# Kernel optimization log

Hardware: AMD Instinct MI355X
Metric: run time of the kernel (lower is better)

The kernel has to match this reference:

```python
import jax, jax.numpy as jnp
import numpy as np

DT = 0.05        # Euler step size
S_EULER = 2      # Euler steps between consecutive events, and after the last one (prop_to_end)


def setup_inputs() -> dict:
    key = jax.random.key(0)
    B, H, D, K, E = 512, 512, 128, 64, 256
    ks = jax.random.split(key, 16)

    def w(k, fan_in, fan_out):
        return jax.random.normal(k, (fan_in, fan_out), jnp.float32) / np.float32(np.sqrt(fan_in))

    X = jax.random.normal(ks[0], (K, E, D), jnp.float32)
    M = jax.random.bernoulli(ks[1], 0.5, (K, E, D)).astype(jnp.float32)
    # unique sample indices per event (irregular observation pattern, no scatter collisions)
    batch_idx = jax.vmap(lambda k: jax.random.permutation(k, B)[:E])(jax.random.split(ks[2], K))
    sample_idx = jnp.arange(B)
    b = lambda n: jnp.full((n,), 0.01, jnp.float32)  # torch init: bias filled with 0.01
    return {
        'X': X, 'M': M, 'batch_idx': batch_idx, 'sample_idx': sample_idx,
        'Wi': w(ks[3], D + H, H), 'bi': b(H),
        'Wf': w(ks[4], D + H, H), 'bf': b(H),
        'Wo': w(ks[5], D + H, H), 'bo': b(H),
        'Wc': w(ks[6], D + H, H), 'bc': b(H),
        'W1': w(ks[7], H, H), 'b1': b(H),
        'W2': w(ks[8], H, H), 'b2': b(H),
        'Wp1': w(ks[9], H, H), 'bp1': b(H),
        'Wp2': w(ks[10], H, D), 'bp2': b(D),
    }


def reference(X, M, batch_idx, sample_idx,
              Wi, bi, Wf, bf, Wo, bo, Wc, bc,
              W1, b1, W2, b2, Wp1, bp1, Wp2, bp2):
    B = sample_idx.shape[0]
    H = W1.shape[0]
    h0 = jnp.zeros((B, H), X.dtype)
    c0 = jnp.zeros((B, H), X.dtype)

    def euler(h):  # h <- h + dt * ODEFunc(h)
        return h + DT * (jnp.tanh(h @ W1 + b1) @ W2 + b2)

    def p_model(h):  # Linear -> ReLU -> (Dropout p=0, eval) -> Linear
        return jax.nn.relu(h @ Wp1 + bp1) @ Wp2 + bp2

    def step(carry, xs):
        h, c, loss, tot_m = carry
        Xo, Mo, idx = xs  # [E,D], [E,D], [E]
        for _ in range(S_EULER):
            h = euler(h)
        p = p_model(h)
        loss = loss + jnp.sum(jnp.abs(Xo - p[idx]) * Mo)
        tot_m = tot_m + jnp.sum(Mo)
        inp = jnp.concatenate([Xo, h[idx]], axis=-1)  # [E, D+H]
        ig = jax.nn.sigmoid(inp @ Wi + bi)
        fg = jax.nn.sigmoid(inp @ Wf + bf)
        og = jax.nn.sigmoid(inp @ Wo + bo)
        ct = jnp.tanh(inp @ Wc + bc)
        c_new = fg * c[idx] + ig * ct
        h_new = og * jnp.tanh(c_new)
        return (h.at[idx].set(h_new), c.at[idx].set(c_new), loss, tot_m), None

    init = (h0, c0, jnp.float32(0.0), jnp.float32(0.0))
    (h, c, loss, tot_m), _ = jax.lax.scan(step, init, (X, M, batch_idx))
    for _ in range(S_EULER):  # prop_to_end up to T
        h = euler(h)
    return jnp.stack([loss, loss / tot_m])
```

## Files before the change

kernel.cpp:

```cpp
#include <hip/hip_runtime.h>
#include <hip/hip_fp16.h>
#include <stdint.h>

#define Kn 64
#define En 256
#define Bn 512
#define Hn 512
#define Dn 128
#define NBLK 256
#define NTH  256
#define DT_C 0.05f


typedef _Float16 f16x8 __attribute__((ext_vector_type(8)));
typedef float    f32x4 __attribute__((ext_vector_type(4)));
typedef unsigned long long u64;

__device__ __forceinline__ float sigm(float x){ return 1.0f/(1.0f + __expf(-x)); }

__device__ __forceinline__ u64 ald(const u64* p){
  return __hip_atomic_load(p, __ATOMIC_RELAXED, __HIP_MEMORY_SCOPE_AGENT);
}
__device__ __forceinline__ void ast(u64* p, u64 v){
  __hip_atomic_store(p, v, __ATOMIC_RELAXED, __HIP_MEMORY_SCOPE_AGENT);
}

union HU { __half h[8]; u64 q[2]; uint32_t w[4]; };

__global__ void k_init(int* __restrict__ pos, float* __restrict__ acc,
                       int* __restrict__ ctr, uint32_t* __restrict__ hf){
  int i = blockIdx.x*blockDim.x + threadIdx.x;
  if (i < Kn*Bn) pos[i] = -1;
  if (i < 2) acc[i] = 0.0f;
  if (i < 1024) ctr[i] = 0;
  if (i < Hn*Hn/2) hf[i] = 0;
}

__global__ void k_scatter(const int* __restrict__ bidx, int* __restrict__ pos){
  int i = blockIdx.x*blockDim.x + threadIdx.x;
  if (i < Kn*En){
    int k = i >> 8;
    int e = i & (En-1);
    pos[(k << 9) | bidx[i]] = e;
  }
}

__global__ void k_cvt_frag(const float* __restrict__ src, __half* __restrict__ dst,
                           int KT, int N, int n){
  int i = blockIdx.x*blockDim.x + threadIdx.x;
  if (i >= n) return;
  int C = i / (KT*512);
  int r = i % (KT*512);
  int T = r >> 9;
  int q = r & 511;
  int l = q >> 3, e = q & 7;
  int srow = T*32 + ((l>>4)<<3) + e;
  int scol = C*16 + (l&15);
  dst[i] = __float2half(src[(size_t)srow*N + scol]);
}

__device__ __forceinline__ void gsync(int* c, int tgt){
  asm volatile("s_waitcnt vmcnt(0)" ::: "memory");
  __syncthreads();
  if (threadIdx.x == 0){
    __hip_atomic_fetch_add(c, 1, __ATOMIC_RELAXED, __HIP_MEMORY_SCOPE_AGENT);
    while (__hip_atomic_load(c, __ATOMIC_RELAXED, __HIP_MEMORY_SCOPE_AGENT) < tgt)
      __builtin_amdgcn_s_sleep(1);
  }
  __syncthreads();
}

__global__ __launch_bounds__(NTH, 1) void k_main(
  const float* __restrict__ X, const float* __restrict__ Mm,
  const int* __restrict__ pos, const __half* __restrict__ WF,
  __half* __restrict__ Hf, __half* __restrict__ Tf,
  const float* __restrict__ bi_, const float* __restrict__ bf_,
  const float* __restrict__ bo_, const float* __restrict__ bc_,
  const float* __restrict__ b1_, const float* __restrict__ b2_,
  const float* __restrict__ bp1_, const float* __restrict__ bp2_,
  float* __restrict__ acc, int* __restrict__ ctrbase)
{
  const __half* W1F  = WF;
  const __half* W2F  = WF + 262144;
  const __half* Wp1F = WF + 524288;
  const __half* Wp2F = WF + 786432;
  const __half* WgF  = WF + 851968;

  const int t    = threadIdx.x;
  const int bid  = blockIdx.x;
  const int s    = bid & 7;
  const int g    = bid >> 3;
  const int w    = t >> 6;
  const int lane = t & 63;

  int* ctr = ctrbase + g*32;

  __shared__ __align__(16) __half Afrag[16*512];
  __shared__ __align__(16) __half Xfrag[4*512];
  __shared__ __align__(16) float  outb[20*256];
  __shared__ float redbuf[8];

  const int row = t >> 4;
  const int q4  = t & 15;
  const int sc  = s*64 + q4*4;
  float Hreg[4] = {0,0,0,0};
  float Creg[4] = {0,0,0,0};
  float vb1[4], vb2[4], vbp1[4], vbi[4], vbf[4], vbo[4], vbc[4];
  #pragma unroll
  for (int i=0;i<4;i++){
    vb1[i]=b1_[sc+i]; vb2[i]=b2_[sc+i]; vbp1[i]=bp1_[sc+i];
    vbi[i]=bi_[sc+i]; vbf[i]=bf_[sc+i]; vbo[i]=bo_[sc+i]; vbc[i]=bc_[sc+i];
  }
  const float vbp2 = bp2_[s*16 + q4];

  f16x8 W1r[16], W2r[16], Wp1r[16];
  {
    const size_t cb = (size_t)(s*4 + w)*16*512 + lane*8;
    #pragma unroll
    for (int kt=0; kt<16; kt++){
      W1r[kt]  = *(const f16x8*)(W1F  + cb + kt*512);
      W2r[kt]  = *(const f16x8*)(W2F  + cb + kt*512);
      Wp1r[kt] = *(const f16x8*)(Wp1F + cb + kt*512);
    }
  }

  float loss_loc = 0.f, m_loc = 0.f;
  int round = 0;
  const int grow = g*16 + row;

  for (int k=0; k<Kn; k++){
    const int epos = pos[(k<<9) + grow];

    #pragma unroll 1
    for (int ph=0; ph<4; ph++){
      const __half* src = (ph & 1) ? Tf : Hf;
      {
        const int ar = t & 15, ch = t >> 4;
        const u64* sp = (const u64*)(src + ((size_t)(g*16+ar))*512 + ch*32);
        u64 v[8];
        #pragma unroll
        for (int i=0;i<8;i++) v[i] = ald(sp+i);
        #pragma unroll
        for (int kg=0;kg<4;kg++){
          u64* d = (u64*)(Afrag + ch*512 + (ar + 16*kg)*8);
          d[0] = v[2*kg]; d[1] = v[2*kg+1];
        }
      }
      __syncthreads();
      {
        f32x4 a4 = {0,0,0,0};
        if (!(ph & 1)){
          #pragma unroll
          for (int kt=0; kt<16; kt++){
            f16x8 a = *(const f16x8*)(Afrag + kt*512 + lane*8);
            a4 = __builtin_amdgcn_mfma_f32_16x16x32_f16(a, W1r[kt], a4, 0,0,0);
          }
        } else {
          #pragma unroll
          for (int kt=0; kt<16; kt++){
            f16x8 a = *(const f16x8*)(Afrag + kt*512 + lane*8);
            a4 = __builtin_amdgcn_mfma_f32_16x16x32_f16(a, W2r[kt], a4, 0,0,0);
          }
        }
        float* o = outb + w*256 + ((lane>>4)*4)*16 + (lane&15);
        o[0]=a4[0]; o[16]=a4[1]; o[32]=a4[2]; o[48]=a4[3];
      }
      __syncthreads();
      {
        const float* o = outb + (q4>>2)*256 + row*16 + (q4&3)*4;
        float v0=o[0], v1=o[1], v2=o[2], v3=o[3];
        HU u;
        if (!(ph & 1)){
          u.h[0]=__float2half(tanhf(v0+vb1[0])); u.h[1]=__float2half(tanhf(v1+vb1[1]));
          u.h[2]=__float2half(tanhf(v2+vb1[2])); u.h[3]=__float2half(tanhf(v3+vb1[3]));
          ast((u64*)(Tf + (size_t)grow*512 + sc), u.q[0]);
        } else {
          Hreg[0] += DT_C*(v0+vb2[0]); Hreg[1] += DT_C*(v1+vb2[1]);
          Hreg[2] += DT_C*(v2+vb2[2]); Hreg[3] += DT_C*(v3+vb2[3]);
          u.h[0]=__float2half(Hreg[0]); u.h[1]=__float2half(Hreg[1]);
          u.h[2]=__float2half(Hreg[2]); u.h[3]=__float2half(Hreg[3]);
          ast((u64*)(Hf + (size_t)grow*512 + sc), u.q[0]);
        }
      }
      gsync(ctr, 8*(++round));
    }

    {
      {
        const int ar = t & 15, ch = t >> 4;
        const u64* sp = (const u64*)(Hf + ((size_t)(g*16+ar))*512 + ch*32);
        u64 v[8];
        #pragma unroll
        for (int i=0;i<8;i++) v[i] = ald(sp+i);
        #pragma unroll
        for (int kg=0;kg<4;kg++){
          u64* d = (u64*)(Afrag + ch*512 + (ar + 16*kg)*8);
          d[0] = v[2*kg]; d[1] = v[2*kg+1];
        }
      }
      if (t < 64){
        const int ar = t & 15, ch = t >> 4;
        const int e = pos[(k<<9) + g*16 + ar];
        float xv[32];
        if (e >= 0){
          const float4* xp = (const float4*)(X + ((size_t)(k*En+e))*Dn + ch*32);
          #pragma unroll
          for (int i=0;i<8;i++){
            float4 f = xp[i];
            xv[4*i]=f.x; xv[4*i+1]=f.y; xv[4*i+2]=f.z; xv[4*i+3]=f.w;
          }
        } else {
          #pragma unroll
          for (int i=0;i<32;i++) xv[i]=0.f;
        }
        #pragma unroll
        for (int kg=0;kg<4;kg++){
          HU u;
          #pragma unroll
          for (int e8=0;e8<8;e8++) u.h[e8] = __float2half(xv[kg*8+e8]);
          u64* d = (u64*)(Xfrag + ch*512 + (ar + 16*kg)*8);
          d[0] = u.q[0]; d[1] = u.q[1];
        }
      }
      __syncthreads();
      {
        f32x4 a4 = {0,0,0,0};
        #pragma unroll
        for (int kt=0; kt<16; kt++){
          f16x8 a = *(const f16x8*)(Afrag + kt*512 + lane*8);
          a4 = __builtin_amdgcn_mfma_f32_16x16x32_f16(a, Wp1r[kt], a4, 0,0,0);
        }
        float* o = outb + (16+w)*256 + ((lane>>4)*4)*16 + (lane&15);
        o[0]=a4[0]; o[16]=a4[1]; o[32]=a4[2]; o[48]=a4[3];
      }
      #pragma unroll 1
      for (int i=0;i<4;i++){
        const int Cg = w*32 + s*4 + i;
        const __half* wb = WgF + (size_t)Cg*20*512;
        f32x4 a4 = {0,0,0,0};
        #pragma unroll 4
        for (int kt=0; kt<4; kt++){
          f16x8 a = *(const f16x8*)(Xfrag + kt*512 + lane*8);
          f16x8 b = *(const f16x8*)(wb + kt*512 + lane*8);
          a4 = __builtin_amdgcn_mfma_f32_16x16x32_f16(a, b, a4, 0,0,0);
        }
        #pragma unroll 4
        for (int kt=4; kt<20; kt++){
          f16x8 a = *(const f16x8*)(Afrag + (kt-4)*512 + lane*8);
          f16x8 b = *(const f16x8*)(wb + kt*512 + lane*8);
          a4 = __builtin_amdgcn_mfma_f32_16x16x32_f16(a, b, a4, 0,0,0);
        }
        float* o = outb + (w*4+i)*256 + ((lane>>4)*4)*16 + (lane&15);
        o[0]=a4[0]; o[16]=a4[1]; o[32]=a4[2]; o[48]=a4[3];
      }
      __syncthreads();
      {
        const float* o = outb + (16+(q4>>2))*256 + row*16 + (q4&3)*4;
        HU u;
        u.h[0]=__float2half(fmaxf(o[0]+vbp1[0],0.f));
        u.h[1]=__float2half(fmaxf(o[1]+vbp1[1],0.f));
        u.h[2]=__float2half(fmaxf(o[2]+vbp1[2],0.f));
        u.h[3]=__float2half(fmaxf(o[3]+vbp1[3],0.f));
        ast((u64*)(Tf + (size_t)grow*512 + sc), u.q[0]);
      }
      gsync(ctr, 8*(++round));
    }

    {
      {
        const int ar = t & 15, ch = t >> 4;
        const u64* sp = (const u64*)(Tf + ((size_t)(g*16+ar))*512 + ch*32);
        u64 v[8];
        #pragma unroll
        for (int i=0;i<8;i++) v[i] = ald(sp+i);
        #pragma unroll
        for (int kg=0;kg<4;kg++){
          u64* d = (u64*)(Afrag + ch*512 + (ar + 16*kg)*8);
          d[0] = v[2*kg]; d[1] = v[2*kg+1];
        }
      }
      __syncthreads();
      {
        const __half* wb = Wp2F + (size_t)s*16*512;
        f32x4 a4 = {0,0,0,0};
        #pragma unroll
        for (int kt2=0; kt2<4; kt2++){
          const int kt = w*4 + kt2;
          f16x8 a = *(const f16x8*)(Afrag + kt*512 + lane*8);
          f16x8 b = *(const f16x8*)(wb + kt*512 + lane*8);
          a4 = __builtin_amdgcn_mfma_f32_16x16x32_f16(a, b, a4, 0,0,0);
        }
        float* o = outb + (16+w)*256 + ((lane>>4)*4)*16 + (lane&15);
        o[0]=a4[0]; o[16]=a4[1]; o[32]=a4[2]; o[48]=a4[3];
      }
      if (epos >= 0){
        const int sub = q4 >> 2, off = row*16 + (q4&3)*4;
        const float4 pi = *(const float4*)(outb + (0*4+sub)*256 + off);
        const float4 pf = *(const float4*)(outb + (1*4+sub)*256 + off);
        const float4 po = *(const float4*)(outb + (2*4+sub)*256 + off);
        const float4 pc = *(const float4*)(outb + (3*4+sub)*256 + off);
        HU hu;
        const float gi[4]={pi.x,pi.y,pi.z,pi.w}, gf[4]={pf.x,pf.y,pf.z,pf.w};
        const float go[4]={po.x,po.y,po.z,po.w}, gc[4]={pc.x,pc.y,pc.z,pc.w};
        #pragma unroll
        for (int i=0;i<4;i++){
          float ig = sigm(gi[i] + vbi[i]);
          float fg = sigm(gf[i] + vbf[i]);
          float og = sigm(go[i] + vbo[i]);
          float ct = tanhf(gc[i] + vbc[i]);
          Creg[i] = fg*Creg[i] + ig*ct;
          Hreg[i] = og*tanhf(Creg[i]);
          hu.h[i] = __float2half(Hreg[i]);
        }
        ast((u64*)(Hf + (size_t)grow*512 + sc), hu.q[0]);
      }
      __syncthreads();
      if (epos >= 0){
        float p = outb[16*256 + row*16+q4] + outb[17*256 + row*16+q4]
                + outb[18*256 + row*16+q4] + outb[19*256 + row*16+q4] + vbp2;
        const int d = s*16 + q4;
        float xo = X[((size_t)(k*En+epos))*Dn + d];
        float mo = Mm[((size_t)(k*En+epos))*Dn + d];
        loss_loc += fabsf(xo - p)*mo;
        m_loc    += mo;
      }
      gsync(ctr, 8*(++round));
    }
  }

  #pragma unroll
  for (int off=32; off>0; off>>=1){
    loss_loc += __shfl_down(loss_loc, off);
    m_loc    += __shfl_down(m_loc, off);
  }
  if (lane == 0){ redbuf[w] = loss_loc; redbuf[4+w] = m_loc; }
  __syncthreads();
  if (t == 0){
    atomicAdd(acc+0, redbuf[0]+redbuf[1]+redbuf[2]+redbuf[3]);
    atomicAdd(acc+1, redbuf[4]+redbuf[5]+redbuf[6]+redbuf[7]);
  }
}

__global__ void k_fin(const float* __restrict__ acc, float* __restrict__ out){
  if (threadIdx.x == 0){
    out[0] = acc[0];
    out[1] = acc[0]/acc[1];
  }
}

extern "C" void kernel_launch(void* const* d_in, const int* in_sizes, int n_in,
                              void* d_out, int out_size, void* d_ws, size_t ws_size,
                              hipStream_t stream)
{
  const float* X   = (const float*)d_in[0];
  const float* Mm  = (const float*)d_in[1];
  const int*  bidx = (const int*)d_in[2];
  const float* Wi  = (const float*)d_in[4];
  const float* bi  = (const float*)d_in[5];
  const float* Wf  = (const float*)d_in[6];
  const float* bff = (const float*)d_in[7];
  const float* Wo  = (const float*)d_in[8];
  const float* bo  = (const float*)d_in[9];
  const float* Wc  = (const float*)d_in[10];
  const float* bc  = (const float*)d_in[11];
  const float* W1  = (const float*)d_in[12];
  const float* b1  = (const float*)d_in[13];
  const float* W2  = (const float*)d_in[14];
  const float* b2  = (const float*)d_in[15];
  const float* Wp1 = (const float*)d_in[16];
  const float* bp1 = (const float*)d_in[17];
  const float* Wp2 = (const float*)d_in[18];
  const float* bp2 = (const float*)d_in[19];

  char* ws = (char*)d_ws;
  int*    pos = (int*)ws;
  float*  acc = (float*)(ws + 131072);
  int*    ctr = (int*)(ws + 131200);
  __half* Hf  = (__half*)(ws + 1048576);
  __half* Tf  = (__half*)(ws + 1572864);
  __half* WF  = (__half*)(ws + 4194304);

  k_init   <<<512, 256, 0, stream>>>(pos, acc, ctr, (uint32_t*)Hf);
  k_scatter<<<(Kn*En + 255)/256, 256, 0, stream>>>(bidx, pos);

  k_cvt_frag<<<(262144+255)/256, 256, 0, stream>>>(W1,  WF,          16, 512, 262144);
  k_cvt_frag<<<(262144+255)/256, 256, 0, stream>>>(W2,  WF + 262144, 16, 512, 262144);
  k_cvt_frag<<<(262144+255)/256, 256, 0, stream>>>(Wp1, WF + 524288, 16, 512, 262144);
  k_cvt_frag<<<(65536 +255)/256, 256, 0, stream>>>(Wp2, WF + 786432, 16, 128, 65536);
  k_cvt_frag<<<(327680+255)/256, 256, 0, stream>>>(Wi,  WF + 851968,            20, 512, 327680);
  k_cvt_frag<<<(327680+255)/256, 256, 0, stream>>>(Wf,  WF + 851968 + 327680,   20, 512, 327680);
  k_cvt_frag<<<(327680+255)/256, 256, 0, stream>>>(Wo,  WF + 851968 + 655360,   20, 512, 327680);
  k_cvt_frag<<<(327680+255)/256, 256, 0, stream>>>(Wc,  WF + 851968 + 983040,   20, 512, 327680);

  k_main<<<NBLK, NTH, 0, stream>>>(X, Mm, pos, WF, Hf, Tf,
                                   bi, bff, bo, bc, b1, b2, bp1, bp2, acc, ctr);
  k_fin<<<1, 64, 0, stream>>>(acc, (float*)d_out);
}
```

Before: 1.916 ms.

## Restructure recurrent kernel with split-K partial sums and per-block flag barriers

Adds a new main kernel that keeps each block-group's full hidden state in shared memory. The W2 product is computed as split-K partial sums that every block exchanges and reduces locally. This cuts grid-wide barriers from about five per event to three, and the barrier becomes per-block flag stores instead of a shared counter. The prediction loss is deferred to the next event, and only updated LSTM rows are exchanged. The cost is more global traffic for the partial sums, more shared memory, and a larger workspace requirement, with a fallback to the old kernel when the workspace is too small.

```diff
diff --git a/kernel.cpp b/kernel.cpp
--- a/kernel.cpp
+++ b/kernel.cpp
@@ -11,6 +11,7 @@
 #define NTH  256
 #define DT_C 0.05f
 
+#define WS_NEED_PS 19660800ULL
 
 typedef _Float16 f16x8 __attribute__((ext_vector_type(8)));
 typedef float    f32x4 __attribute__((ext_vector_type(4)));
@@ -24,15 +25,23 @@
 __device__ __forceinline__ void ast(u64* p, u64 v){
   __hip_atomic_store(p, v, __ATOMIC_RELAXED, __HIP_MEMORY_SCOPE_AGENT);
 }
-
-union HU { __half h[8]; u64 q[2]; uint32_t w[4]; };
+__device__ __forceinline__ uint32_t ald32(const uint32_t* p){
+  return __hip_atomic_load(p, __ATOMIC_RELAXED, __HIP_MEMORY_SCOPE_AGENT);
+}
+__device__ __forceinline__ void ast32(uint32_t* p, uint32_t v){
+  __hip_atomic_store(p, v, __ATOMIC_RELAXED, __HIP_MEMORY_SCOPE_AGENT);
+}
+
+union HU { __half h[8]; u64 q[2]; };
 
 __global__ void k_init(int* __restrict__ pos, float* __restrict__ acc,
-                       int* __restrict__ ctr, uint32_t* __restrict__ hf){
+                       int* __restrict__ ctr, int* __restrict__ flg,
+                       uint32_t* __restrict__ hf){
   int i = blockIdx.x*blockDim.x + threadIdx.x;
   if (i < Kn*Bn) pos[i] = -1;
   if (i < 2) acc[i] = 0.0f;
   if (i < 1024) ctr[i] = 0;
+  if (i < 8192) flg[i] = 0;
   if (i < Hn*Hn/2) hf[i] = 0;
 }
 
@@ -59,7 +68,352 @@
   dst[i] = __float2half(src[(size_t)srow*N + scol]);
 }
 
-__device__ __forceinline__ void gsync(int* c, int tgt){
+__device__ __forceinline__ f32x4 mv16(const __half* Af, const f16x8* Wr, int lane){
+  f32x4 a = {0.f,0.f,0.f,0.f};
+  #pragma unroll
+  for (int kt=0; kt<16; kt++){
+    f16x8 av = *(const f16x8*)(Af + kt*512 + lane*8);
+    a = __builtin_amdgcn_mfma_f32_16x16x32_f16(av, Wr[kt], a, 0,0,0);
+  }
+  return a;
+}
+
+__global__ __launch_bounds__(NTH, 1) void k_main_ps(
+  const float* __restrict__ X, const float* __restrict__ Mm,
+  const int* __restrict__ pos, const __half* __restrict__ WF,
+  __half* __restrict__ Qb, float* __restrict__ Rb, __half* __restrict__ Hp,
+  const float* __restrict__ bi_, const float* __restrict__ bf_,
+  const float* __restrict__ bo_, const float* __restrict__ bc_,
+  const float* __restrict__ b1_, const float* __restrict__ b2_,
+  const float* __restrict__ bp1_, const float* __restrict__ bp2_,
+  float* __restrict__ acc, int* __restrict__ flg)
+{
+  const __half* W1F  = WF;
+  const __half* W2F  = WF + 262144;
+  const __half* Wp1F = WF + 524288;
+  const __half* Wp2F = WF + 786432;
+  const __half* WgF  = WF + 851968;
+
+  const int t    = threadIdx.x;
+  const int bid  = blockIdx.x;
+  const int s    = bid & 7;
+  const int g    = bid >> 3;
+  const int w    = t >> 6;
+  const int lane = t & 63;
+  int* flgbase = flg + g*8*32;
+
+  __shared__ __align__(16) __half Afrag[8192];
+  __shared__ __align__(16) __half Xfrag[2048];
+  __shared__ __align__(16) __half T1sm[1024];
+  __shared__ __align__(16) float  hm[8192];
+  __shared__ __align__(16) float  outg[4096];
+  __shared__ __align__(16) __half outq[8192];
+  __shared__ float b2s[512];
+  __shared__ int   posk[16];
+  __shared__ float redbuf[8];
+
+  const float vb1r  = b1_ [s*64 + w*16 + (lane&15)];
+  const float vbp1r = bp1_[s*64 + w*16 + (lane&15)];
+  const float vbp2  = bp2_[s*16 + (t&15)];
+  float vbi[4], vbf[4], vbo[4], vbc[4];
+  #pragma unroll
+  for (int j=0;j<4;j++){
+    const int c = s*64 + (t&15)*4 + j;
+    vbi[j]=bi_[c]; vbf[j]=bf_[c]; vbo[j]=bo_[c]; vbc[j]=bc_[c];
+  }
+  float Creg[4] = {0,0,0,0};
+
+  f16x8 W1r[16], W2r[16], Wp1r[16], Wp2r[4];
+  {
+    #pragma unroll
+    for (int kt=0; kt<16; kt++){
+      W1r[kt]  = *(const f16x8*)(W1F  + (size_t)((s*4+w)*16 + kt)*512 + lane*8);
+      Wp1r[kt] = *(const f16x8*)(Wp1F + (size_t)((s*4+w)*16 + kt)*512 + lane*8);
+    }
+    #pragma unroll
+    for (int c2=0;c2<8;c2++)
+      #pragma unroll
+      for (int j=0;j<2;j++)
+        W2r[c2*2+j] = *(const f16x8*)(W2F + (size_t)((w*8+c2)*16 + 2*s + j)*512 + lane*8);
+    #pragma unroll
+    for (int c2=0;c2<2;c2++)
+      #pragma unroll
+      for (int j=0;j<2;j++)
+        Wp2r[c2*2+j] = *(const f16x8*)(Wp2F + (size_t)((w*2+c2)*16 + 2*s + j)*512 + lane*8);
+  }
+
+  for (int i=t;i<8192;i+=NTH){ hm[i]=0.f; Afrag[i]=__float2half(0.f); }
+  for (int i=t;i<512;i+=NTH) b2s[i]=b2_[i];
+  __syncthreads();
+
+  float loss_loc=0.f, m_loc=0.f;
+  int rnd = 0;
+
+#define QSLOT(G,ST,R) (((size_t)(G)*2 + (ST))*8 + (R))*8192
+
+#define GSYNC() do{                                                          \
+    asm volatile("s_waitcnt vmcnt(0)" ::: "memory");                         \
+    __syncthreads();                                                         \
+    rnd++;                                                                   \
+    if (t == 0)                                                              \
+      __hip_atomic_store(flgbase + s*32, rnd, __ATOMIC_RELAXED,              \
+                         __HIP_MEMORY_SCOPE_AGENT);                          \
+    if (t < 8){                                                              \
+      while (__hip_atomic_load(flgbase + t*32, __ATOMIC_RELAXED,             \
+                               __HIP_MEMORY_SCOPE_AGENT) < rnd)              \
+        __builtin_amdgcn_s_sleep(1);                                         \
+    }                                                                        \
+    __syncthreads();                                                         \
+  }while(0)
+
+#define EULER_STEP(ST) do{                                                   \
+    f32x4 a1 = mv16(Afrag, W1r, lane);                                       \
+    _Pragma("unroll")                                                        \
+    for (int i=0;i<4;i++)                                                    \
+      T1sm[((lane>>4)*4+i)*64 + w*16 + (lane&15)] =                          \
+        __float2half(tanhf(a1[i]+vb1r));                                     \
+    __syncthreads();                                                         \
+    f32x4 qa[8];                                                             \
+    _Pragma("unroll") for (int c2=0;c2<8;c2++) qa[c2]=(f32x4){0,0,0,0};      \
+    _Pragma("unroll")                                                        \
+    for (int j=0;j<2;j++){                                                   \
+      f16x8 av = *(const f16x8*)(T1sm + (lane&15)*64 + j*32 + (lane>>4)*8);  \
+      _Pragma("unroll")                                                      \
+      for (int c2=0;c2<8;c2++)                                               \
+        qa[c2] = __builtin_amdgcn_mfma_f32_16x16x32_f16(av, W2r[c2*2+j],     \
+                                                        qa[c2], 0,0,0);      \
+    }                                                                        \
+    _Pragma("unroll")                                                        \
+    for (int c2=0;c2<8;c2++){                                                \
+      const int col = (w*8+c2)*16 + (lane&15);                               \
+      _Pragma("unroll")                                                      \
+      for (int i=0;i<4;i++)                                                  \
+        outq[((lane>>4)*4+i)*512 + col] = __float2half(qa[c2][i]);           \
+    }                                                                        \
+    __syncthreads();                                                         \
+    { const int qL=t&15, kt=t>>4;                                            \
+      u64* dst = (u64*)(Qb + QSLOT(g,(ST),s) + kt*512 + qL*32);              \
+      _Pragma("unroll")                                                      \
+      for (int li=0;li<4;li++){                                              \
+        const int L=qL*4+li;                                                 \
+        const u64* sp = (const u64*)(outq + (L&15)*512 + kt*32 + (L>>4)*8);  \
+        ast(dst+li*2,   sp[0]);                                              \
+        ast(dst+li*2+1, sp[1]);                                              \
+      } }                                                                    \
+    GSYNC();                                                                 \
+  }while(0)
+
+#define REDUCE(ST) do{                                                       \
+    const int qL=t&15, kt=t>>4;                                              \
+    float sum[32];                                                           \
+    _Pragma("unroll") for (int i=0;i<32;i++) sum[i]=0.f;                     \
+    _Pragma("unroll")                                                        \
+    for (int r=0;r<8;r++){                                                   \
+      const u64* qp = (const u64*)(Qb + QSLOT(g,(ST),r) + kt*512 + qL*32);   \
+      u64 vv[8];                                                             \
+      _Pragma("unroll") for (int i=0;i<8;i++) vv[i]=ald(qp+i);               \
+      _Pragma("unroll")                                                      \
+      for (int li=0;li<4;li++){                                              \
+        _Pragma("unroll")                                                    \
+        for (int h2=0;h2<2;h2++){                                            \
+          u64 xx = vv[li*2+h2];                                              \
+          _Pragma("unroll")                                                  \
+          for (int e=0;e<4;e++)                                              \
+            sum[li*8+h2*4+e] +=                                              \
+              __half2float(__ushort_as_half((unsigned short)(xx>>(16*e))));  \
+        } } }                                                                \
+    _Pragma("unroll")                                                        \
+    for (int li=0;li<4;li++){                                                \
+      const int L=qL*4+li, row=L&15, kb=kt*32+(L>>4)*8;                      \
+      _Pragma("unroll")                                                      \
+      for (int e=0;e<8;e++){                                                 \
+        float nh = hm[row*512+kb+e] + DT_C*(sum[li*8+e] + b2s[kb+e]);        \
+        hm[row*512+kb+e]=nh;                                                 \
+        Afrag[kt*512+L*8+e]=__float2half(nh);                                \
+      } }                                                                    \
+    __syncthreads();                                                         \
+  }while(0)
+
+  for (int k=0; k<Kn; k++){
+    if (k > 0){
+      {
+        const int lrow=t>>4, q4=t&15;
+        const int ep = posk[lrow];
+        if (ep >= 0){
+          float p = vbp2;
+          #pragma unroll
+          for (int r=0;r<8;r++)
+            p += __uint_as_float(ald32((const uint32_t*)Rb +
+                   (size_t)(g*8+r)*2048 + s*256 + lrow*16 + q4));
+          const size_t xo = ((size_t)((k-1)*En+ep))*Dn + s*16 + q4;
+          float mo = Mm[xo];
+          loss_loc += fabsf(X[xo]-p)*mo; m_loc += mo;
+        }
+      }
+      {
+        const int qL=t&15, kt=t>>4, r=kt>>1, kt2=kt&1;
+        const u64* hp = (const u64*)(Hp + (size_t)(g*8+r)*1024 + kt2*512 + qL*32);
+        #pragma unroll
+        for (int li=0;li<4;li++){
+          const int L=qL*4+li, row=L&15;
+          if (posk[row] >= 0){
+            u64 lo = ald(hp + li*2), hi2 = ald(hp + li*2 + 1);
+            #pragma unroll
+            for (int e=0;e<4;e++){
+              __half hv = __ushort_as_half((unsigned short)(lo >> (16*e)));
+              hm[row*512 + kt*32 + (L>>4)*8 + e] = __half2float(hv);
+              Afrag[kt*512 + L*8 + e] = hv;
+            }
+            #pragma unroll
+            for (int e=0;e<4;e++){
+              __half hv = __ushort_as_half((unsigned short)(hi2 >> (16*e)));
+              hm[row*512 + kt*32 + (L>>4)*8 + 4 + e] = __half2float(hv);
+              Afrag[kt*512 + L*8 + 4 + e] = hv;
+            }
+          }
+        }
+      }
+      __syncthreads();
+    }
+    EULER_STEP(0);
+
+    REDUCE(0);
+    EULER_STEP(1);
+
+    REDUCE(1);
+    if (t < 16) posk[t] = pos[(k<<9) + g*16 + t];
+    if (t < 64){
+      const int ar = t & 15, ch = t >> 4;
+      const int e = pos[(k<<9) + g*16 + ar];
+      float xv[32];
+      if (e >= 0){
+        const float4* xp = (const float4*)(X + ((size_t)(k*En+e))*Dn + ch*32);
+        #pragma unroll
+        for (int i=0;i<8;i++){
+          float4 f = xp[i];
+          xv[4*i]=f.x; xv[4*i+1]=f.y; xv[4*i+2]=f.z; xv[4*i+3]=f.w;
+        }
+      } else {
+        #pragma unroll
+        for (int i=0;i<32;i++) xv[i]=0.f;
+      }
+      #pragma unroll
+      for (int kg=0;kg<4;kg++){
+        HU u;
+        #pragma unroll
+        for (int e8=0;e8<8;e8++) u.h[e8] = __float2half(xv[kg*8+e8]);
+        u64* d = (u64*)(Xfrag + ch*512 + (ar + 16*kg)*8);
+        d[0] = u.q[0]; d[1] = u.q[1];
+      }
+    }
+    {
+      f32x4 p1 = mv16(Afrag, Wp1r, lane);
+      #pragma unroll
+      for (int i=0;i<4;i++)
+        T1sm[((lane>>4)*4+i)*64 + w*16 + (lane&15)] =
+          __float2half(fmaxf(p1[i]+vbp1r, 0.f));
+    }
+    __syncthreads();
+    #pragma unroll
+    for (int c2=0;c2<2;c2++){
+      f32x4 a4 = {0,0,0,0};
+      #pragma unroll
+      for (int j=0;j<2;j++){
+        f16x8 av = *(const f16x8*)(T1sm + (lane&15)*64 + j*32 + (lane>>4)*8);
+        a4 = __builtin_amdgcn_mfma_f32_16x16x32_f16(av, Wp2r[c2*2+j], a4, 0,0,0);
+      }
+      const int ct = w*2 + c2;
+      uint32_t* rb = (uint32_t*)Rb + (size_t)(g*8+s)*2048 + ct*256 + (lane&15);
+      #pragma unroll
+      for (int i=0;i<4;i++)
+        ast32(rb + ((lane>>4)*4+i)*16, __float_as_uint(a4[i]));
+    }
+    if (k < Kn-1){
+      #pragma unroll 1
+      for (int i4=0;i4<4;i4++){
+        const int Cg = w*32 + s*4 + i4;
+        const __half* wb = WgF + (size_t)Cg*20*512;
+        f32x4 a4 = {0,0,0,0};
+        #pragma unroll 4
+        for (int kt=0;kt<4;kt++){
+          f16x8 av = *(const f16x8*)(Xfrag + kt*512 + lane*8);
+          f16x8 bv = *(const f16x8*)(wb + kt*512 + lane*8);
+          a4 = __builtin_amdgcn_mfma_f32_16x16x32_f16(av, bv, a4, 0,0,0);
+        }
+        #pragma unroll 4
+        for (int kt=4;kt<20;kt++){
+          f16x8 av = *(const f16x8*)(Afrag + (kt-4)*512 + lane*8);
+          f16x8 bv = *(const f16x8*)(wb + kt*512 + lane*8);
+          a4 = __builtin_amdgcn_mfma_f32_16x16x32_f16(av, bv, a4, 0,0,0);
+        }
+        #pragma unroll
+        for (int i=0;i<4;i++)
+          outg[w*1024 + ((lane>>4)*4+i)*64 + i4*16 + (lane&15)] = a4[i];
+      }
+      __syncthreads();
+      {
+        const int lrow=t>>4, q4=t&15;
+        const int eo = posk[lrow];
+        unsigned short hb[4];
+        if (eo >= 0){
+          #pragma unroll
+          for (int j=0;j<4;j++){
+            const int col = q4*4+j;
+            float pi = outg[0*1024 + lrow*64 + col];
+            float pf = outg[1*1024 + lrow*64 + col];
+            float po = outg[2*1024 + lrow*64 + col];
+            float pc = outg[3*1024 + lrow*64 + col];
+            float ig=sigm(pi+vbi[j]), fg=sigm(pf+vbf[j]);
+            float og=sigm(po+vbo[j]), ctv=tanhf(pc+vbc[j]);
+            Creg[j] = fg*Creg[j] + ig*ctv;
+            hb[j] = __half_as_ushort(__float2half(og*tanhf(Creg[j])));
+          }
+        } else {
+          #pragma unroll
+          for (int j=0;j<4;j++)
+            hb[j] = __half_as_ushort(__float2half(hm[lrow*512 + s*64 + q4*4 + j]));
+        }
+        u64 pk = (u64)hb[0] | ((u64)hb[1]<<16) | ((u64)hb[2]<<32) | ((u64)hb[3]<<48);
+        const int kt2=q4>>3, ln=lrow+16*((q4&7)>>1), e0=(q4*4)&7;
+        ast((u64*)(Hp + (size_t)(g*8+s)*1024 + kt2*512 + ln*8 + e0), pk);
+      }
+    }
+    GSYNC();
+  }
+
+  {
+    const int lrow=t>>4, q4=t&15;
+    const int ep = posk[lrow];
+    if (ep >= 0){
+      float p = vbp2;
+      #pragma unroll
+      for (int r=0;r<8;r++)
+        p += __uint_as_float(ald32((const uint32_t*)Rb +
+               (size_t)(g*8+r)*2048 + s*256 + lrow*16 + q4));
+      const size_t xo = ((size_t)((Kn-1)*En+ep))*Dn + s*16 + q4;
+      float mo = Mm[xo];
+      loss_loc += fabsf(X[xo]-p)*mo; m_loc += mo;
+    }
+  }
+
+  #pragma unroll
+  for (int off=32; off>0; off>>=1){
+    loss_loc += __shfl_down(loss_loc, off);
+    m_loc    += __shfl_down(m_loc, off);
+  }
+  if (lane == 0){ redbuf[w] = loss_loc; redbuf[4+w] = m_loc; }
+  __syncthreads();
+  if (t == 0){
+    atomicAdd(acc+0, redbuf[0]+redbuf[1]+redbuf[2]+redbuf[3]);
+    atomicAdd(acc+1, redbuf[4]+redbuf[5]+redbuf[6]+redbuf[7]);
+  }
+#undef QSLOT
+#undef GSYNC
+#undef EULER_STEP
+#undef REDUCE
+}
+
+__device__ __forceinline__ void gsync7(int* c, int tgt){
   asm volatile("s_waitcnt vmcnt(0)" ::: "memory");
   __syncthreads();
   if (threadIdx.x == 0){
@@ -70,7 +424,7 @@
   __syncthreads();
 }
 
-__global__ __launch_bounds__(NTH, 1) void k_main(
+__global__ __launch_bounds__(NTH, 1) void k_main_r7(
   const float* __restrict__ X, const float* __restrict__ Mm,
   const int* __restrict__ pos, const __half* __restrict__ WF,
   __half* __restrict__ Hf, __half* __restrict__ Tf,
@@ -92,7 +446,6 @@
   const int g    = bid >> 3;
   const int w    = t >> 6;
   const int lane = t & 63;
-
   int* ctr = ctrbase + g*32;
 
   __shared__ __align__(16) __half Afrag[16*512];
@@ -115,7 +468,7 @@
 
   f16x8 W1r[16], W2r[16], Wp1r[16];
   {
-    const size_t cb = (size_t)(s*4 + w)*16*512 + lane*8;
+    const size_t cb = (size_t)(s*4 + w)*16*512 + (size_t)lane*8;
     #pragma unroll
     for (int kt=0; kt<16; kt++){
       W1r[kt]  = *(const f16x8*)(W1F  + cb + kt*512);
@@ -128,15 +481,14 @@
   int round = 0;
   const int grow = g*16 + row;
 
-  for (int k=0; k<Kn; k++){
+  for (int k=0;k<Kn;k++){
     const int epos = pos[(k<<9) + grow];
-
     #pragma unroll 1
     for (int ph=0; ph<4; ph++){
-      const __half* src = (ph & 1) ? Tf : Hf;
+      const __half* srcb = (ph & 1) ? Tf : Hf;
       {
         const int ar = t & 15, ch = t >> 4;
-        const u64* sp = (const u64*)(src + ((size_t)(g*16+ar))*512 + ch*32);
+        const u64* sp = (const u64*)(srcb + ((size_t)(g*16+ar))*512 + ch*32);
         u64 v[8];
         #pragma unroll
         for (int i=0;i<8;i++) v[i] = ald(sp+i);
@@ -149,19 +501,8 @@
       __syncthreads();
       {
         f32x4 a4 = {0,0,0,0};
-        if (!(ph & 1)){
-          #pragma unroll
-          for (int kt=0; kt<16; kt++){
-            f16x8 a = *(const f16x8*)(Afrag + kt*512 + lane*8);
-            a4 = __builtin_amdgcn_mfma_f32_16x16x32_f16(a, W1r[kt], a4, 0,0,0);
-          }
-        } else {
-          #pragma unroll
-          for (int kt=0; kt<16; kt++){
-            f16x8 a = *(const f16x8*)(Afrag + kt*512 + lane*8);
-            a4 = __builtin_amdgcn_mfma_f32_16x16x32_f16(a, W2r[kt], a4, 0,0,0);
-          }
-        }
+        if (!(ph & 1)) a4 = mv16(Afrag, W1r, lane);
+        else           a4 = mv16(Afrag, W2r, lane);
         float* o = outb + w*256 + ((lane>>4)*4)*16 + (lane&15);
         o[0]=a4[0]; o[16]=a4[1]; o[32]=a4[2]; o[48]=a4[3];
       }
@@ -182,9 +523,8 @@
           ast((u64*)(Hf + (size_t)grow*512 + sc), u.q[0]);
         }
       }
-      gsync(ctr, 8*(++round));
-    }
-
+      gsync7(ctr, 8*(++round));
+    }
     {
       {
         const int ar = t & 15, ch = t >> 4;
@@ -224,12 +564,7 @@
       }
       __syncthreads();
       {
-        f32x4 a4 = {0,0,0,0};
-        #pragma unroll
-        for (int kt=0; kt<16; kt++){
-          f16x8 a = *(const f16x8*)(Afrag + kt*512 + lane*8);
-          a4 = __builtin_amdgcn_mfma_f32_16x16x32_f16(a, Wp1r[kt], a4, 0,0,0);
-        }
+        f32x4 a4 = mv16(Afrag, Wp1r, lane);
         float* o = outb + (16+w)*256 + ((lane>>4)*4)*16 + (lane&15);
         o[0]=a4[0]; o[16]=a4[1]; o[32]=a4[2]; o[48]=a4[3];
       }
@@ -263,9 +598,8 @@
         u.h[3]=__float2half(fmaxf(o[3]+vbp1[3],0.f));
         ast((u64*)(Tf + (size_t)grow*512 + sc), u.q[0]);
       }
-      gsync(ctr, 8*(++round));
-    }
-
+      gsync7(ctr, 8*(++round));
+    }
     {
       {
         const int ar = t & 15, ch = t >> 4;
@@ -324,7 +658,7 @@
         loss_loc += fabsf(xo - p)*mo;
         m_loc    += mo;
       }
-      gsync(ctr, 8*(++round));
+      gsync7(ctr, 8*(++round));
     }
   }
 
@@ -376,11 +710,15 @@
   int*    pos = (int*)ws;
   float*  acc = (float*)(ws + 131072);
   int*    ctr = (int*)(ws + 131200);
+  int*    flg = (int*)(ws + 196608);
   __half* Hf  = (__half*)(ws + 1048576);
   __half* Tf  = (__half*)(ws + 1572864);
   __half* WF  = (__half*)(ws + 4194304);
-
-  k_init   <<<512, 256, 0, stream>>>(pos, acc, ctr, (uint32_t*)Hf);
+  __half* Qb  = (__half*)(ws + 8650752);
+  float*  Rb  = (float*)(ws + 17039360);
+  __half* Hp  = (__half*)(ws + 19136512);
+
+  k_init   <<<512, 256, 0, stream>>>(pos, acc, ctr, flg, (uint32_t*)Hf);
   k_scatter<<<(Kn*En + 255)/256, 256, 0, stream>>>(bidx, pos);
 
   k_cvt_frag<<<(262144+255)/256, 256, 0, stream>>>(W1,  WF,          16, 512, 262144);
@@ -392,7 +730,12 @@
   k_cvt_frag<<<(327680+255)/256, 256, 0, stream>>>(Wo,  WF + 851968 + 655360,   20, 512, 327680);
   k_cvt_frag<<<(327680+255)/256, 256, 0, stream>>>(Wc,  WF + 851968 + 983040,   20, 512, 327680);
 
-  k_main<<<NBLK, NTH, 0, stream>>>(X, Mm, pos, WF, Hf, Tf,
-                                   bi, bff, bo, bc, b1, b2, bp1, bp2, acc, ctr);
+  if (ws_size >= WS_NEED_PS){
+    k_main_ps<<<NBLK, NTH, 0, stream>>>(X, Mm, pos, WF, Qb, Rb, Hp,
+                                        bi, bff, bo, bc, b1, b2, bp1, bp2, acc, flg);
+  } else {
+    k_main_r7<<<NBLK, NTH, 0, stream>>>(X, Mm, pos, WF, Hf, Tf,
+                                        bi, bff, bo, bc, b1, b2, bp1, bp2, acc, ctr);
+  }
   k_fin<<<1, 64, 0, stream>>>(acc, (float*)d_out);
 }
```

New measurement: 5.055 ms. +163.8%, slower.
